# Optimization experiments

Measured on AMD Instinct MI355X. Metric: run time of the kernel, lower is better.

## Reference

```python
import jax, jax.numpy as jnp
import numpy as np

B, NB, T, NC = 32, 55, 512, 8
D, H, E, K, DEPTH, FF = 128, 8, 8, 2, 4, 512  # embed, heads, experts, top_k, depth, ffn hidden=4*D
IN = NB * NC  # 440


def _ln(x, g, b, eps=1e-5):
    m = jnp.mean(x, axis=-1, keepdims=True)
    v = jnp.mean((x - m) ** 2, axis=-1, keepdims=True)
    return (x - m) / jnp.sqrt(v + eps) * g + b


def setup_inputs() -> dict:
    key = jax.random.key(0)
    ks = jax.random.split(key, 16)
    s = 0.02
    return {
        "x": jax.random.normal(ks[0], (B, NB, T, NC), jnp.float32),
        "proj_W": jax.random.normal(ks[1], (IN, D), jnp.float32) * s,
        "proj_b": jnp.zeros((D,), jnp.float32),
        "pos_embed": jax.random.normal(ks[2], (1, T, D), jnp.float32) * s,
        "ln1_g": jnp.ones((DEPTH, D), jnp.float32),
        "ln1_b": jnp.zeros((DEPTH, D), jnp.float32),
        "qkv_W": jax.random.normal(ks[3], (DEPTH, D, 3 * D), jnp.float32) * s,
        "qkv_b": jnp.zeros((DEPTH, 3 * D), jnp.float32),
        "out_W": jax.random.normal(ks[4], (DEPTH, D, D), jnp.float32) * s,
        "out_b": jnp.zeros((DEPTH, D), jnp.float32),
        "ln2_g": jnp.ones((DEPTH, D), jnp.float32),
        "ln2_b": jnp.zeros((DEPTH, D), jnp.float32),
        "gate_W": jax.random.normal(ks[5], (DEPTH, D, E), jnp.float32) * s,
        "w1": jax.random.normal(ks[6], (DEPTH, E, D, FF), jnp.float32) * s,
        "b1": jnp.zeros((DEPTH, E, FF), jnp.float32),
        "w2": jax.random.normal(ks[7], (DEPTH, E, FF, D), jnp.float32) * s,
        "b2": jnp.zeros((DEPTH, E, D), jnp.float32),
        "head_ln_g": jnp.ones((D,), jnp.float32),
        "head_ln_b": jnp.zeros((D,), jnp.float32),
        "head_W": jax.random.normal(ks[8], (D, 2), jnp.float32) * s,
        "head_b": jnp.zeros((2,), jnp.float32),
    }


def reference(x, proj_W, proj_b, pos_embed, ln1_g, ln1_b, qkv_W, qkv_b, out_W,
              out_b, ln2_g, ln2_b, gate_W, w1, b1, w2, b2, head_ln_g,
              head_ln_b, head_W, head_b):
    b, nb, t, nc = x.shape
    h = jnp.transpose(x, (0, 2, 1, 3)).reshape(b, t, nb * nc)  # [b,t,440]
    h = h @ proj_W + proj_b + pos_embed[:, :t, :]
    aux_total = jnp.float32(0.0)
    for i in range(DEPTH):
        # --- pre-LN multi-head self-attention ---
        z = _ln(h, ln1_g[i], ln1_b[i])
        qkv = z @ qkv_W[i] + qkv_b[i]
        q, k, v = jnp.split(qkv, 3, axis=-1)
        dh = D // H
        q = q.reshape(b, t, H, dh)
        k = k.reshape(b, t, H, dh)
        v = v.reshape(b, t, H, dh)
        att = jnp.einsum('bqhd,bkhd->bhqk', q, k) / jnp.sqrt(jnp.float32(dh))
        att = jax.nn.softmax(att, axis=-1)
        o = jnp.einsum('bhqk,bkhd->bqhd', att, v).reshape(b, t, D)
        h = h + o @ out_W[i] + out_b[i]
        # --- pre-LN top-k MoE FFN ---
        z = _ln(h, ln2_g[i], ln2_b[i])
        probs = jax.nn.softmax(z @ gate_W[i], axis=-1)  # [b,t,E]
        topv, topi = jax.lax.top_k(probs, K)
        wts = topv / jnp.sum(topv, axis=-1, keepdims=True)
        combine = jnp.sum(jax.nn.one_hot(topi, E, dtype=probs.dtype) * wts[..., None], axis=-2)  # [b,t,E]
        hid = jax.nn.gelu(jnp.einsum('btd,edf->btef', z, w1[i]) + b1[i])
        yexp = jnp.einsum('btef,efd->bted', hid, w2[i]) + b2[i]
        h = h + jnp.einsum('bte,bted->btd', combine, yexp)
        # Switch-style load-balancing auxiliary loss
        importance = probs.mean(axis=(0, 1))            # mean router prob per expert
        load = (combine > 0).astype(probs.dtype).mean(axis=(0, 1))  # dispatch fraction
        aux_total = aux_total + E * jnp.sum(importance * load)
    pooled = h.mean(axis=1)
    pooled = _ln(pooled, head_ln_g, head_ln_b)
    return pooled @ head_W + head_b, aux_total
```

## Files before the change

kernel.cpp:

```cpp
#include <hip/hip_runtime.h>
#include <hip/hip_bf16.h>
#include <cstdint>
#include <cstddef>

#define BT        16384
#define MAXASSIGN 33792
#define QSCALE    0.36067376022224085f

typedef __attribute__((ext_vector_type(8)))  short short8;
typedef __attribute__((ext_vector_type(4)))  short short4v;
typedef __attribute__((ext_vector_type(4)))  float f32x4;
typedef __attribute__((ext_vector_type(16))) float f32x16;

typedef const uint32_t __attribute__((address_space(1))) gas_u32;
typedef uint32_t __attribute__((address_space(3))) las_u32;

__device__ __forceinline__ void gload16(const void* g, void* l) {
    __builtin_amdgcn_global_load_lds((gas_u32*)g, (las_u32*)l, 16, 0, 0);
}

__device__ __forceinline__ float gelu_f(float x) {
    float u2l = (x + 0.044715f * x * x * x) * 2.3022081927f;
    float e = exp2f(u2l);
    float r = __builtin_amdgcn_rcpf(e + 1.0f);
    return x * e * r;
}

__device__ __forceinline__ unsigned pkbf(float a, float b) {
    __hip_bfloat16 ha = __float2bfloat16(a);
    __hip_bfloat16 hb = __float2bfloat16(b);
    unsigned short ua = *reinterpret_cast<unsigned short*>(&ha);
    unsigned short ub = *reinterpret_cast<unsigned short*>(&hb);
    return (unsigned)ua | ((unsigned)ub << 16);
}

__global__ __launch_bounds__(256) void transpose_kernel(const float* __restrict__ x,
                                                        __hip_bfloat16* __restrict__ xtb) {
    __shared__ unsigned tile[64][228];
    const int b  = blockIdx.x >> 3;
    const int t0 = (blockIdx.x & 7) * 64;
    const int tid = threadIdx.x;
    tile[tid >> 2][220 + (tid & 3)] = 0u;
    const int tt  = tid >> 2;
    const int ncp = tid & 3;
    for (int nb = 0; nb < 55; ++nb) {
        const float2* src = (const float2*)(x + (((size_t)(b * 55 + nb)) * 512 + t0) * 8);
        float2 v = src[tid];
        tile[tt][nb * 4 + ncp] = pkbf(v.x, v.y);
    }
    __syncthreads();
#pragma unroll
    for (int u = 0; u < 14; ++u) {
        int idx = u * 256 + tid;
        int t = idx / 56, c = idx % 56;
        *(uint4*)(xtb + ((size_t)b * 512 + t0 + t) * 448 + c * 8) =
            *(const uint4*)&tile[t][c * 4];
    }
}

__global__ __launch_bounds__(256) void wconvt_kernel(const float* __restrict__ in,
                                                     __hip_bfloat16* __restrict__ out,
                                                     int K, int N) {
    __shared__ float tile[64][65];
    const int kt = K >> 6, nt = N >> 6;
    const int per = kt * nt;
    const int bb  = blockIdx.x / per;
    const int rem = blockIdx.x % per;
    const int k0  = (rem / nt) << 6;
    const int n0  = (rem % nt) << 6;
    const int tid = threadIdx.x;

    const float* src = in + ((size_t)bb * K + k0) * N + n0;
    int tk = tid >> 4;
    int tn = (tid & 15) * 4;
#pragma unroll
    for (int r = 0; r < 4; ++r) {
        float4 v = *(const float4*)(src + (size_t)(tk + r * 16) * N + tn);
        tile[tk + r * 16][tn]     = v.x;
        tile[tk + r * 16][tn + 1] = v.y;
        tile[tk + r * 16][tn + 2] = v.z;
        tile[tk + r * 16][tn + 3] = v.w;
    }
    __syncthreads();
    int on = tid >> 2;
    int ok = (tid & 3) * 16;
    unsigned pk[8];
#pragma unroll
    for (int u = 0; u < 8; ++u)
        pk[u] = pkbf(tile[ok + 2 * u][on], tile[ok + 2 * u + 1][on]);
    uint4* dst = (uint4*)(out + ((size_t)bb * N + n0 + on) * K + k0 + ok);
    dst[0] = (uint4){pk[0], pk[1], pk[2], pk[3]};
    dst[1] = (uint4){pk[4], pk[5], pk[6], pk[7]};
}

__global__ __launch_bounds__(256) void projconv_kernel(const float* __restrict__ in,
                                                       __hip_bfloat16* __restrict__ out) {
    int idx = blockIdx.x * 256 + threadIdx.x;
    int k = idx % 448, n = idx / 448;
    out[idx] = __float2bfloat16(k < 440 ? in[k * 128 + n] : 0.f);
}

template<int MODE, int BM>
__global__ __launch_bounds__(256) void mm_kernel(
    const __hip_bfloat16* __restrict__ A, const __hip_bfloat16* __restrict__ Wt,
    const float* __restrict__ bias, const float* __restrict__ extra,
    void* __restrict__ Cout, int K, int N, int wstride,
    const int* __restrict__ moff, const int* __restrict__ atok,
    const float* __restrict__ awt)
{
    constexpr int FI = BM / 32;
    __shared__ short smem[16384];
    short* As = smem;
    short* Bs = smem + BM * 64;
    const int tid  = threadIdx.x;
    const int row0 = blockIdx.x * BM;
    const int col0 = blockIdx.y * 128;

    const float* bias2 = bias;
    int lim = 0;
    if constexpr (MODE == 3 || MODE == 4) {
        if (row0 >= moff[8]) return;
        int e = 0;
        while (moff[e + 1] <= row0) ++e;
        Wt    += (size_t)e * wstride;
        bias2  = bias + e * N;
        lim    = moff[e] + moff[9 + e];
    }

    const int wave = tid >> 6, lane = tid & 63;
    const int crow = tid >> 3;
    const int cc   = tid & 7;

    int srow[FI];
#pragma unroll
    for (int p = 0; p < FI; ++p) {
        int grow = row0 + p * 32 + crow;
        srow[p] = grow;
        if constexpr (MODE == 3)
            srow[p] = (grow < lim) ? atok[grow] : BT;
    }

    f32x4 acc[FI][4];
#pragma unroll
    for (int i = 0; i < FI; ++i)
#pragma unroll
        for (int j = 0; j < 4; ++j) acc[i][j] = (f32x4){0.f, 0.f, 0.f, 0.f};

    const int wm = (wave >> 1) * (BM / 2), wn = (wave & 1) * 64;
    const int lr = lane & 15, q = lane >> 4;

    for (int k0 = 0; k0 < K; k0 += 64) {
#pragma unroll
        for (int p = 0; p < FI; ++p) {
            int row = p * 32 + crow;
            int sc  = (cc ^ (row & 7)) << 3;
            short* la = &As[(p * 32 + wave * 8) * 64];
            gload16(A + (size_t)srow[p] * K + k0 + sc, la);
        }
#pragma unroll
        for (int p = 0; p < 4; ++p) {
            int row = p * 32 + crow;
            int sc  = (cc ^ (row & 7)) << 3;
            short* lb = &Bs[(p * 32 + wave * 8) * 64];
            gload16(Wt + (size_t)(col0 + row) * K + k0 + sc, lb);
        }
        __syncthreads();
#pragma unroll
        for (int s = 0; s < 2; ++s) {
            short8 af[FI], bf[4];
#pragma unroll
            for (int f = 0; f < FI; ++f) {
                int m = wm + f * 16 + lr;
                af[f] = *(const short8*)&As[(m * 8 + ((s * 4 + q) ^ (m & 7))) * 8];
            }
#pragma unroll
            for (int f = 0; f < 4; ++f) {
                int n = wn + f * 16 + lr;
                bf[f] = *(const short8*)&Bs[(n * 8 + ((s * 4 + q) ^ (n & 7))) * 8];
            }
#pragma unroll
            for (int i = 0; i < FI; ++i)
#pragma unroll
                for (int j = 0; j < 4; ++j)
                    acc[i][j] = __builtin_amdgcn_mfma_f32_16x16x32_bf16(
                        bf[j], af[i], acc[i][j], 0, 0, 0);
        }
        __syncthreads();
    }

    float4 b4[4];
#pragma unroll
    for (int j = 0; j < 4; ++j)
        b4[j] = *(const float4*)&bias2[col0 + wn + j * 16 + q * 4];

    if constexpr (MODE == 3 || MODE == 5) {
        const bool qsc = (MODE == 5) && (col0 == 0);
#pragma unroll
        for (int i = 0; i < FI; ++i) {
            int trow = wm + i * 16 + lr;
#pragma unroll
            for (int j = 0; j < 4; ++j) {
                int cb = wn + j * 16 + q * 4;
                float v0 = acc[i][j][0] + b4[j].x;
                float v1 = acc[i][j][1] + b4[j].y;
                float v2 = acc[i][j][2] + b4[j].z;
                float v3 = acc[i][j][3] + b4[j].w;
                if constexpr (MODE == 3) {
                    v0 = gelu_f(v0); v1 = gelu_f(v1);
                    v2 = gelu_f(v2); v3 = gelu_f(v3);
                }
                if (qsc) { v0 *= QSCALE; v1 *= QSCALE; v2 *= QSCALE; v3 *= QSCALE; }
                uint2 pk = {pkbf(v0, v1), pkbf(v2, v3)};
                int ch = cb >> 3;
                *(uint2*)((char*)smem + trow * 256 + ((ch ^ (trow & 7)) << 4)
                          + ((cb & 7) << 1)) = pk;
            }
        }
        __syncthreads();
        __hip_bfloat16* outb = (__hip_bfloat16*)Cout;
        constexpr int TPR = 256 / BM;
        constexpr int CPT = 16 / TPR;
        int rrow = tid / TPR;
        if constexpr (MODE == 3) {
            size_t rb = (size_t)(row0 + rrow) * N + col0;
#pragma unroll
            for (int u = 0; u < CPT; ++u) {
                int c = (tid % TPR) * CPT + u;
                uint4 d = *(const uint4*)((char*)smem + rrow * 256
                                          + ((c ^ (rrow & 7)) << 4));
                *(uint4*)(outb + rb + c * 8) = d;
            }
        } else {
            size_t pbase = (size_t)(col0 >> 7) * 8 * BT * 16;
#pragma unroll
            for (int u = 0; u < CPT; ++u) {
                int c = (tid % TPR) * CPT + u;
                uint4 d = *(const uint4*)((char*)smem + rrow * 256
                                          + ((c ^ (rrow & 7)) << 4));
                size_t dst = pbase + ((size_t)(c >> 1) * BT + row0 + rrow) * 16
                           + (c & 1) * 8;
                *(uint4*)(outb + dst) = d;
            }
        }
    } else {
        float* outf = (float*)Cout;
        constexpr int HP = BM / 64;
        for (int h = 0; h < HP; ++h) {
            if (HP == 1 || (wm >> 6) == h) {
#pragma unroll
                for (int i = 0; i < FI; ++i) {
                    int trow = (wm & 63) + i * 16 + lr;
#pragma unroll
                    for (int j = 0; j < 4; ++j) {
                        int cb = wn + j * 16 + q * 4;
                        f32x4 v = acc[i][j];
                        v[0] += b4[j].x; v[1] += b4[j].y;
                        v[2] += b4[j].z; v[3] += b4[j].w;
                        int ch = cb >> 2;
                        *(f32x4*)((char*)smem + trow * 512
                                  + ((ch ^ (trow & 7)) << 4)) = v;
                    }
                }
            }
            __syncthreads();
            {
                int rrow = tid >> 2;
                int grow = row0 + h * 64 + rrow;
                float aw = (MODE == 4) ? awt[grow] : 1.f;
                size_t rb = (size_t)grow * N + col0;
#pragma unroll
                for (int u = 0; u < 8; ++u) {
                    int c = (tid & 3) * 8 + u;
                    f32x4 d = *(const f32x4*)((char*)smem + rrow * 512
                                              + ((c ^ (rrow & 7)) << 4));
                    int gcol = col0 + c * 4;
                    if constexpr (MODE == 0) {
                        float4 p = *(const float4*)&extra[(grow & 511) * 128 + gcol];
                        d[0] += p.x; d[1] += p.y; d[2] += p.z; d[3] += p.w;
                    } else if constexpr (MODE == 2) {
                        float4 p = *(const float4*)&extra[rb + c * 4];
                        d[0] += p.x; d[1] += p.y; d[2] += p.z; d[3] += p.w;
                    } else if constexpr (MODE == 4) {
                        d[0] *= aw; d[1] *= aw; d[2] *= aw; d[3] *= aw;
                    }
                    *(f32x4*)&outf[rb + c * 4] = d;
                }
            }
            __syncthreads();
        }
    }
}

__global__ __launch_bounds__(256) void ln_kernel(const float* __restrict__ x,
                                                 const float* __restrict__ g,
                                                 const float* __restrict__ b,
                                                 __hip_bfloat16* __restrict__ zbf) {
    int wave = threadIdx.x >> 6, lane = threadIdx.x & 63;
    size_t row = (size_t)blockIdx.x * 4 + wave;
    const float* xr = x + row * 128;
    float a0 = xr[lane], a1 = xr[lane + 64];
    float s = a0 + a1;
#pragma unroll
    for (int off = 32; off > 0; off >>= 1) s += __shfl_xor(s, off);
    float mean = s * (1.f / 128.f);
    float d0 = a0 - mean, d1 = a1 - mean;
    float v = d0 * d0 + d1 * d1;
#pragma unroll
    for (int off = 32; off > 0; off >>= 1) v += __shfl_xor(v, off);
    float inv = rsqrtf(v * (1.f / 128.f) + 1e-5f);
    zbf[row * 128 + lane]      = __float2bfloat16(d0 * inv * g[lane] + b[lane]);
    zbf[row * 128 + lane + 64] = __float2bfloat16(d1 * inv * g[lane + 64] + b[lane + 64]);
}

__global__ __launch_bounds__(512) void attn_kernel(const __hip_bfloat16* __restrict__ qkv,
                                                   __hip_bfloat16* __restrict__ o) {
    __shared__ short Ks[512 * 24];
    __shared__ short Vt[17 * 520];
    const int b = blockIdx.z, hh = blockIdx.y, half = blockIdx.x;
    const int tid = threadIdx.x;
    const __hip_bfloat16* Qh = qkv + ((size_t)(0 * 8 + hh) * BT + b * 512) * 16;
    const __hip_bfloat16* Kh = qkv + ((size_t)(1 * 8 + hh) * BT + b * 512) * 16;
    const __hip_bfloat16* Vh = qkv + ((size_t)(2 * 8 + hh) * BT + b * 512) * 16;

    {
        int r = tid;
        const uint4* ksrc = (const uint4*)(Kh + (size_t)r * 16);
        uint4 k0 = ksrc[0], k1 = ksrc[1];
        *(uint4*)&Ks[r * 24 + 0] = k0;
        *(uint4*)&Ks[r * 24 + 8] = k1;
        const uint4* vsrc = (const uint4*)(Vh + (size_t)r * 16);
        uint4 v0 = vsrc[0], v1 = vsrc[1];
        unsigned vv[8] = {v0.x, v0.y, v0.z, v0.w, v1.x, v1.y, v1.z, v1.w};
#pragma unroll
        for (int c = 0; c < 8; ++c) {
            Vt[(2 * c)     * 520 + r] = (short)(vv[c] & 0xffff);
            Vt[(2 * c + 1) * 520 + r] = (short)(vv[c] >> 16);
        }
        Vt[16 * 520 + r] = (short)0x3F80;
    }
    __syncthreads();

    const int wave = tid >> 6, lane = tid & 63;
    const int lm = lane & 31, lh = lane >> 5;
    const int qrow0 = half * 256 + wave * 32;

    short8 qf = *(const short8*)(Qh + (size_t)(qrow0 + lm) * 16 + lh * 8);

    f32x16 accO;
#pragma unroll
    for (int r = 0; r < 16; ++r) accO[r] = 0.f;

    for (int kc = 0; kc < 16; ++kc) {
        short8 kf = *(const short8*)&Ks[(kc * 32 + lm) * 24 + lh * 8];
        int vr = (lm < 16) ? lm : 16;
        const short* vb2 = &Vt[vr * 520 + kc * 32];
        short4v va  = *(const short4v*)(vb2 + 4 * lh);
        short4v vbq = *(const short4v*)(vb2 + 8 + 4 * lh);
        short4v vc  = *(const short4v*)(vb2 + 16 + 4 * lh);
        short4v vd  = *(const short4v*)(vb2 + 24 + 4 * lh);
        short8 vf0, vf1;
#pragma unroll
        for (int j = 0; j < 4; ++j) {
            vf0[j] = va[j];  vf0[4 + j] = vbq[j];
            vf1[j] = vc[j];  vf1[4 + j] = vd[j];
        }
        f32x16 st;
#pragma unroll
        for (int r = 0; r < 16; ++r) st[r] = 0.f;
        st = __builtin_amdgcn_mfma_f32_32x32x16_bf16(kf, qf, st, 0, 0, 0);
        short8 pf0, pf1;
#pragma unroll
        for (int r = 0; r < 8; ++r) {
            pf0[r] = (short)(__float_as_uint(exp2f(st[r]))     >> 16);
            pf1[r] = (short)(__float_as_uint(exp2f(st[8 + r])) >> 16);
        }
        accO = __builtin_amdgcn_mfma_f32_32x32x16_bf16(pf0, vf0, accO, 0, 0, 0);
        accO = __builtin_amdgcn_mfma_f32_32x32x16_bf16(pf1, vf1, accO, 0, 0, 0);
    }

#pragma unroll
    for (int r = 0; r < 16; ++r) {
        float val = accO[r];
        float s = __shfl(val, (lane & 32) + 16);
        if (lm < 16) {
            int qr = qrow0 + (r & 3) + 8 * (r >> 2) + 4 * lh;
            o[((size_t)b * 512 + qr) * 128 + hh * 16 + lm] = __float2bfloat16(val / s);
        }
    }
}

__global__ __launch_bounds__(256) void ln2gate_kernel(
    const float* __restrict__ x, const float* __restrict__ g, const float* __restrict__ b,
    const float* __restrict__ gW, __hip_bfloat16* __restrict__ zbf,
    int* __restrict__ topi, float* __restrict__ topw,
    float* __restrict__ impS, int* __restrict__ cntS)
{
    __shared__ float simp[8];
    __shared__ int scnt[8];
    const int tid = threadIdx.x;
    if (tid < 8) { simp[tid] = 0.f; scnt[tid] = 0; }
    __syncthreads();
    const int wave = tid >> 6, lane = tid & 63;
    const size_t row = (size_t)blockIdx.x * 4 + wave;
    const float* xr = x + row * 128;
    float a0 = xr[lane], a1 = xr[lane + 64];
    float s = a0 + a1;
#pragma unroll
    for (int off = 32; off > 0; off >>= 1) s += __shfl_xor(s, off);
    float mean = s * (1.f / 128.f);
    float d0 = a0 - mean, d1 = a1 - mean;
    float v = d0 * d0 + d1 * d1;
#pragma unroll
    for (int off = 32; off > 0; off >>= 1) v += __shfl_xor(v, off);
    float inv = rsqrtf(v * (1.f / 128.f) + 1e-5f);
    float o0 = d0 * inv * g[lane] + b[lane];
    float o1 = d1 * inv * g[lane + 64] + b[lane + 64];
    zbf[row * 128 + lane]      = __float2bfloat16(o0);
    zbf[row * 128 + lane + 64] = __float2bfloat16(o1);
    float4 gA = *(const float4*)&gW[lane * 8];
    float4 gB = *(const float4*)&gW[lane * 8 + 4];
    float4 gC = *(const float4*)&gW[(lane + 64) * 8];
    float4 gD = *(const float4*)&gW[(lane + 64) * 8 + 4];
    float lg[8];
    lg[0] = o0 * gA.x + o1 * gC.x;  lg[1] = o0 * gA.y + o1 * gC.y;
    lg[2] = o0 * gA.z + o1 * gC.z;  lg[3] = o0 * gA.w + o1 * gC.w;
    lg[4] = o0 * gB.x + o1 * gD.x;  lg[5] = o0 * gB.y + o1 * gD.y;
    lg[6] = o0 * gB.z + o1 * gD.z;  lg[7] = o0 * gB.w + o1 * gD.w;
#pragma unroll
    for (int e = 0; e < 8; ++e)
#pragma unroll
        for (int off = 32; off > 0; off >>= 1) lg[e] += __shfl_xor(lg[e], off);
    if (lane == 0) {
        float p[8];
        float mx = lg[0];
#pragma unroll
        for (int k = 1; k < 8; ++k) mx = fmaxf(mx, lg[k]);
        float ssum = 0.f;
#pragma unroll
        for (int k = 0; k < 8; ++k) { p[k] = expf(lg[k] - mx); ssum += p[k]; }
        float pinv = 1.f / ssum;
#pragma unroll
        for (int k = 0; k < 8; ++k) p[k] *= pinv;
        int i0 = 0; float v0 = p[0];
#pragma unroll
        for (int k = 1; k < 8; ++k) if (p[k] > v0) { v0 = p[k]; i0 = k; }
        int i1 = -1; float v1 = -1.f;
#pragma unroll
        for (int k = 0; k < 8; ++k) if (k != i0 && p[k] > v1) { v1 = p[k]; i1 = k; }
        float wsum = v0 + v1;
        topi[row * 2] = i0;  topi[row * 2 + 1] = i1;
        topw[row * 2] = v0 / wsum;  topw[row * 2 + 1] = v1 / wsum;
#pragma unroll
        for (int k = 0; k < 8; ++k) atomicAdd(&simp[k], p[k]);
        atomicAdd(&scnt[i0], 1); atomicAdd(&scnt[i1], 1);
    }
    __syncthreads();
    if (tid < 8) {
        int slot = (blockIdx.x & 63) * 8 + tid;
        atomicAdd(&impS[slot], simp[tid]);
        atomicAdd(&cntS[slot], scnt[tid]);
    }
}

__global__ void offsets_kernel(const int* __restrict__ cntS, const float* __restrict__ impS,
                               int* __restrict__ moff, int* __restrict__ fill,
                               float* __restrict__ aux) {
    __shared__ int   csh[8];
    __shared__ float ish[8];
    const int tid = threadIdx.x;
    const int e = tid & 7, grp = tid >> 3;
    int c = 0; float im = 0.f;
    for (int g = 0; g < 8; ++g) {
        int sl = grp * 8 + g;
        c  += cntS[sl * 8 + e];
        im += impS[sl * 8 + e];
    }
#pragma unroll
    for (int off = 32; off >= 8; off >>= 1) {
        c  += __shfl_down(c, off);
        im += __shfl_down(im, off);
    }
    if (tid < 8) { csh[tid] = c; ish[tid] = im; }
    __syncthreads();
    if (tid == 0) {
        int t = 0; float s = 0.f;
        for (int k = 0; k < 8; ++k) {
            int ck = csh[k];
            moff[k] = t; fill[k] = t;
            moff[9 + k] = ck;
            t += (ck + 127) & ~127;
            s += (ish[k] * (1.f / 16384.f)) * ((float)ck * (1.f / 16384.f));
        }
        moff[8] = t;
        aux[0] += 8.f * s;
    }
}

__global__ __launch_bounds__(256) void scatter_kernel(const int* __restrict__ topi,
                                                      const float* __restrict__ topw,
                                                      int* __restrict__ fill, int* __restrict__ atok,
                                                      float* __restrict__ awt, int* __restrict__ tokpos) {
    __shared__ int lcnt[8];
    __shared__ int lbase[8];
    const int tid = threadIdx.x;
    const int token = blockIdx.x * 256 + tid;
    if (tid < 8) lcnt[tid] = 0;
    __syncthreads();
    const int e0 = topi[token * 2], e1 = topi[token * 2 + 1];
    const float w0 = topw[token * 2], w1 = topw[token * 2 + 1];
    const int l0 = atomicAdd(&lcnt[e0], 1);
    const int l1 = atomicAdd(&lcnt[e1], 1);
    __syncthreads();
    if (tid < 8) lbase[tid] = atomicAdd(&fill[tid], lcnt[tid]);
    __syncthreads();
    const int p0 = lbase[e0] + l0;
    const int p1 = lbase[e1] + l1;
    atok[p0] = token;  awt[p0] = w0;  tokpos[token * 2]     = p0;
    atok[p1] = token;  awt[p1] = w1;  tokpos[token * 2 + 1] = p1;
}

__global__ __launch_bounds__(256) void combine_ln_kernel(
    const float* __restrict__ yw, const int* __restrict__ tokpos,
    float* __restrict__ h, const float* __restrict__ g, const float* __restrict__ b,
    __hip_bfloat16* __restrict__ zbf)
{
    const int tid = threadIdx.x;
    const int wave = tid >> 6, lane = tid & 63;
    const size_t row = (size_t)blockIdx.x * 4 + wave;
    const int p0 = tokpos[row * 2], p1 = tokpos[row * 2 + 1];
    float a0 = h[row * 128 + lane]      + yw[(size_t)p0 * 128 + lane]
             + yw[(size_t)p1 * 128 + lane];
    float a1 = h[row * 128 + lane + 64] + yw[(size_t)p0 * 128 + lane + 64]
             + yw[(size_t)p1 * 128 + lane + 64];
    h[row * 128 + lane]      = a0;
    h[row * 128 + lane + 64] = a1;
    if (zbf) {
        float s = a0 + a1;
#pragma unroll
        for (int off = 32; off > 0; off >>= 1) s += __shfl_xor(s, off);
        float mean = s * (1.f / 128.f);
        float d0 = a0 - mean, d1 = a1 - mean;
        float v = d0 * d0 + d1 * d1;
#pragma unroll
        for (int off = 32; off > 0; off >>= 1) v += __shfl_xor(v, off);
        float inv = rsqrtf(v * (1.f / 128.f) + 1e-5f);
        zbf[row * 128 + lane]      = __float2bfloat16(d0 * inv * g[lane] + b[lane]);
        zbf[row * 128 + lane + 64] = __float2bfloat16(d1 * inv * g[lane + 64] + b[lane + 64]);
    }
}

__global__ __launch_bounds__(1024) void head_kernel(const float* __restrict__ h,
                                                    const float* __restrict__ g,
                                                    const float* __restrict__ bb,
                                                    const float* __restrict__ hW,
                                                    const float* __restrict__ hb,
                                                    const float* __restrict__ aux,
                                                    float* __restrict__ out) {
    __shared__ float part[8][128];
    __shared__ float red[128];
    __shared__ float pl[128];
    int b = blockIdx.x, tid = threadIdx.x;
    int c = tid & 127, w = tid >> 7;
    float s = 0.f;
    for (int t = w; t < 512; t += 8) s += h[((size_t)b * 512 + t) * 128 + c];
    part[w][c] = s;
    __syncthreads();
    float pooled = 0.f;
    if (tid < 128) {
#pragma unroll
        for (int k = 0; k < 8; ++k) pooled += part[k][tid];
        pooled *= (1.f / 512.f);
        red[tid] = pooled;
    }
    __syncthreads();
    for (int st = 64; st > 0; st >>= 1) { if (tid < st) red[tid] += red[tid + st]; __syncthreads(); }
    float mean = red[0] * (1.f / 128.f);
    __syncthreads();
    float d = pooled - mean;
    if (tid < 128) red[tid] = d * d;
    __syncthreads();
    for (int st = 64; st > 0; st >>= 1) { if (tid < st) red[tid] += red[tid + st]; __syncthreads(); }
    float var = red[0] * (1.f / 128.f);
    if (tid < 128) pl[tid] = d / sqrtf(var + 1e-5f) * g[tid] + bb[tid];
    __syncthreads();
    if (tid < 2) {
        float acc = hb[tid];
        for (int k = 0; k < 128; ++k) acc += pl[k] * hW[k * 2 + tid];
        out[b * 2 + tid] = acc;
    }
    if (b == 0 && tid == 0) out[64] = aux[0];
}

extern "C" void kernel_launch(void* const* d_in, const int* in_sizes, int n_in,
                              void* d_out, int out_size, void* d_ws, size_t ws_size,
                              hipStream_t stream) {
    (void)in_sizes; (void)n_in; (void)out_size; (void)ws_size;
    const float* x      = (const float*)d_in[0];
    const float* proj_W = (const float*)d_in[1];
    const float* proj_b = (const float*)d_in[2];
    const float* pos    = (const float*)d_in[3];
    const float* ln1_g  = (const float*)d_in[4];
    const float* ln1_b  = (const float*)d_in[5];
    const float* qkv_W  = (const float*)d_in[6];
    const float* qkv_b  = (const float*)d_in[7];
    const float* out_W  = (const float*)d_in[8];
    const float* out_b  = (const float*)d_in[9];
    const float* ln2_g  = (const float*)d_in[10];
    const float* ln2_b  = (const float*)d_in[11];
    const float* gate_W = (const float*)d_in[12];
    const float* w1     = (const float*)d_in[13];
    const float* b1     = (const float*)d_in[14];
    const float* w2     = (const float*)d_in[15];
    const float* b2     = (const float*)d_in[16];
    const float* hl_g   = (const float*)d_in[17];
    const float* hl_b   = (const float*)d_in[18];
    const float* head_W = (const float*)d_in[19];
    const float* head_b = (const float*)d_in[20];
    float* outp = (float*)d_out;

    float* ws = (float*)d_ws;
    size_t off = 0;
    auto alloc = [&](size_t n) { float* p = ws + off; off += (n + 63) & ~(size_t)63; return p; };
    float* hidbf_f = alloc((size_t)MAXASSIGN * 256);
    float* h       = alloc((size_t)BT * 128);
    float* zbf_f   = alloc((size_t)(BT + 1) * 64);
    float* qkvbf_f = alloc((size_t)BT * 192);
    float* obbf_f  = alloc((size_t)BT * 64);
    float* yw      = alloc((size_t)MAXASSIGN * 128);
    float* projWt_f= alloc(128 * 448 / 2);
    float* qkvWt_f = alloc(4 * 384 * 128 / 2);
    float* outWt_f = alloc(4 * 128 * 128 / 2);
    float* w1t_f   = alloc((size_t)32 * 512 * 128 / 2);
    float* w2t_f   = alloc((size_t)32 * 128 * 512 / 2);
    float* topw    = alloc(32768);
    float* awt     = alloc(MAXASSIGN);
    float* impc    = alloc(4096);
    float* auxp    = alloc(1);
    int* topi      = (int*)alloc(32768);
    int* atok      = (int*)alloc(MAXASSIGN);
    int* tokpos    = (int*)alloc(32768);
    int* moff      = (int*)alloc(32);
    int* fill      = (int*)alloc(8);

    __hip_bfloat16* hidbf  = (__hip_bfloat16*)hidbf_f;
    __hip_bfloat16* xtb    = (__hip_bfloat16*)hidbf_f;
    __hip_bfloat16* zbf    = (__hip_bfloat16*)zbf_f;
    __hip_bfloat16* qkvbf  = (__hip_bfloat16*)qkvbf_f;
    __hip_bfloat16* obbf   = (__hip_bfloat16*)obbf_f;
    __hip_bfloat16* projWt = (__hip_bfloat16*)projWt_f;
    __hip_bfloat16* qkvWt  = (__hip_bfloat16*)qkvWt_f;
    __hip_bfloat16* outWt  = (__hip_bfloat16*)outWt_f;
    __hip_bfloat16* w1t    = (__hip_bfloat16*)w1t_f;
    __hip_bfloat16* w2t    = (__hip_bfloat16*)w2t_f;

    hipMemsetAsync(auxp, 0, 4, stream);
    hipMemsetAsync(impc, 0, 16384, stream);
    hipMemsetAsync((char*)zbf + (size_t)BT * 256, 0, 256, stream);

    transpose_kernel<<<256, 256, 0, stream>>>(x, xtb);
    projconv_kernel<<<224, 256, 0, stream>>>(proj_W, projWt);
    wconvt_kernel<<<48, 256, 0, stream>>>(qkv_W, qkvWt, 128, 384);
    wconvt_kernel<<<16, 256, 0, stream>>>(out_W, outWt, 128, 128);
    wconvt_kernel<<<512, 256, 0, stream>>>(w1, w1t, 128, 512);
    wconvt_kernel<<<512, 256, 0, stream>>>(w2, w2t, 512, 128);

    mm_kernel<0, 64><<<dim3(256, 1), 256, 0, stream>>>(
        xtb, projWt, proj_b, pos, h, 448, 128, 0, nullptr, nullptr, nullptr);
    ln_kernel<<<4096, 256, 0, stream>>>(h, ln1_g, ln1_b, zbf);

    for (int i = 0; i < 4; ++i) {
        float* impS = impc + (size_t)i * 1024;
        int*   cntS = (int*)(impc + (size_t)i * 1024 + 512);
        mm_kernel<5, 64><<<dim3(256, 3), 256, 0, stream>>>(
            zbf, qkvWt + (size_t)i * 384 * 128, qkv_b + i * 384, nullptr, qkvbf,
            128, 384, 0, nullptr, nullptr, nullptr);
        attn_kernel<<<dim3(2, 8, 32), 512, 0, stream>>>(qkvbf, obbf);
        mm_kernel<2, 64><<<dim3(256, 1), 256, 0, stream>>>(
            obbf, outWt + (size_t)i * 128 * 128, out_b + i * 128, h, h,
            128, 128, 0, nullptr, nullptr, nullptr);
        ln2gate_kernel<<<4096, 256, 0, stream>>>(h, ln2_g + i * 128, ln2_b + i * 128,
                                                 gate_W + (size_t)i * 128 * 8, zbf,
                                                 topi, topw, impS, cntS);
        offsets_kernel<<<1, 64, 0, stream>>>(cntS, impS, moff, fill, auxp);
        scatter_kernel<<<64, 256, 0, stream>>>(topi, topw, fill, atok, awt, tokpos);
        mm_kernel<3, 128><<<dim3(264, 4), 256, 0, stream>>>(
            zbf, w1t + (size_t)i * 8 * 512 * 128, b1 + (size_t)i * 8 * 512, nullptr,
            hidbf, 128, 512, 512 * 128, moff, atok, awt);
        mm_kernel<4, 64><<<dim3(528, 1), 256, 0, stream>>>(
            hidbf, w2t + (size_t)i * 8 * 128 * 512, b2 + (size_t)i * 8 * 128, nullptr,
            yw, 512, 128, 128 * 512, moff, atok, awt);
        combine_ln_kernel<<<4096, 256, 0, stream>>>(yw, tokpos, h,
                                                    ln1_g + (i + 1 < 4 ? (i + 1) * 128 : 0),
                                                    ln1_b + (i + 1 < 4 ? (i + 1) * 128 : 0),
                                                    (i < 3) ? zbf : (__hip_bfloat16*)nullptr);
    }
    head_kernel<<<32, 1024, 0, stream>>>(h, hl_g, hl_b, head_W, head_b, auxp, outp);
}
```

Measured before the change: 648.0 us.

## Merge setup kernels and fold offset computation into scatter kernel

Replaces three memsets with a single init kernel, merges the proj-weight conversion into the transpose launch, and merges the four weight transpose launches into one. Each layer's separate offsets kernel is removed. The scatter kernel now derives per-block bases deterministically from per-slot counts, which only works because ln2gate slot indexing was changed to blockIdx>>6 so each slot maps to one scatter block. This cuts launch count and serial tiny kernels, at the cost of every scatter block redundantly reducing the count table.

Result: no change. 639.7 us (-1.3%).

```diff
diff --git a/kernel.cpp b/kernel.cpp
--- a/kernel.cpp
+++ b/kernel.cpp
@@ -34,9 +34,25 @@
     return (unsigned)ua | ((unsigned)ub << 16);
 }
 
+__global__ void init_kernel(float* __restrict__ auxp, float* __restrict__ impc,
+                            unsigned* __restrict__ zrow) {
+    int tid = threadIdx.x;
+    if (tid == 0) auxp[0] = 0.f;
+    for (int u = tid; u < 4096; u += 256) impc[u] = 0.f;
+    if (tid < 64) zrow[tid] = 0u;
+}
+
 __global__ __launch_bounds__(256) void transpose_kernel(const float* __restrict__ x,
-                                                        __hip_bfloat16* __restrict__ xtb) {
+                                                        __hip_bfloat16* __restrict__ xtb,
+                                                        const float* __restrict__ projW,
+                                                        __hip_bfloat16* __restrict__ projWt) {
     __shared__ unsigned tile[64][228];
+    if (blockIdx.x >= 256) {
+        int idx = (blockIdx.x - 256) * 256 + threadIdx.x;
+        int k = idx % 448, n = idx / 448;
+        projWt[idx] = __float2bfloat16(k < 440 ? projW[k * 128 + n] : 0.f);
+        return;
+    }
     const int b  = blockIdx.x >> 3;
     const int t0 = (blockIdx.x & 7) * 64;
     const int tid = threadIdx.x;
@@ -58,14 +74,23 @@
     }
 }
 
-__global__ __launch_bounds__(256) void wconvt_kernel(const float* __restrict__ in,
-                                                     __hip_bfloat16* __restrict__ out,
-                                                     int K, int N) {
+__global__ __launch_bounds__(256) void wconvt4_kernel(
+    const float* __restrict__ qkvW, __hip_bfloat16* __restrict__ qkvWt_,
+    const float* __restrict__ outW, __hip_bfloat16* __restrict__ outWt_,
+    const float* __restrict__ w1i, __hip_bfloat16* __restrict__ w1o,
+    const float* __restrict__ w2i, __hip_bfloat16* __restrict__ w2o)
+{
     __shared__ float tile[64][65];
+    const int bid = blockIdx.x;
+    const float* in; __hip_bfloat16* out; int K, N, blk;
+    if (bid < 48)       { in = qkvW; out = qkvWt_; K = 128; N = 384; blk = bid; }
+    else if (bid < 64)  { in = outW; out = outWt_; K = 128; N = 128; blk = bid - 48; }
+    else if (bid < 576) { in = w1i;  out = w1o;    K = 128; N = 512; blk = bid - 64; }
+    else                { in = w2i;  out = w2o;    K = 512; N = 128; blk = bid - 576; }
     const int kt = K >> 6, nt = N >> 6;
     const int per = kt * nt;
-    const int bb  = blockIdx.x / per;
-    const int rem = blockIdx.x % per;
+    const int bb  = blk / per;
+    const int rem = blk % per;
     const int k0  = (rem / nt) << 6;
     const int n0  = (rem % nt) << 6;
     const int tid = threadIdx.x;
@@ -91,13 +116,6 @@
     uint4* dst = (uint4*)(out + ((size_t)bb * N + n0 + on) * K + k0 + ok);
     dst[0] = (uint4){pk[0], pk[1], pk[2], pk[3]};
     dst[1] = (uint4){pk[4], pk[5], pk[6], pk[7]};
-}
-
-__global__ __launch_bounds__(256) void projconv_kernel(const float* __restrict__ in,
-                                                       __hip_bfloat16* __restrict__ out) {
-    int idx = blockIdx.x * 256 + threadIdx.x;
-    int k = idx % 448, n = idx / 448;
-    out[idx] = __float2bfloat16(k < 440 ? in[k * 128 + n] : 0.f);
 }
 
 template<int MODE, int BM>
@@ -456,63 +474,66 @@
     }
     __syncthreads();
     if (tid < 8) {
-        int slot = (blockIdx.x & 63) * 8 + tid;
+        int slot = (blockIdx.x >> 6) * 8 + tid;
         atomicAdd(&impS[slot], simp[tid]);
         atomicAdd(&cntS[slot], scnt[tid]);
     }
 }
 
-__global__ void offsets_kernel(const int* __restrict__ cntS, const float* __restrict__ impS,
-                               int* __restrict__ moff, int* __restrict__ fill,
-                               float* __restrict__ aux) {
-    __shared__ int   csh[8];
-    __shared__ float ish[8];
+__global__ __launch_bounds__(256) void scatter_kernel(
+    const int* __restrict__ topi, const float* __restrict__ topw,
+    const int* __restrict__ cntS, const float* __restrict__ impS,
+    int* __restrict__ atok, float* __restrict__ awt, int* __restrict__ tokpos,
+    int* __restrict__ moffw, float* __restrict__ aux)
+{
+    __shared__ int lcnt[8];
+    __shared__ int lbase[8];
+    __shared__ int csum[8];
+    __shared__ float isum[8];
     const int tid = threadIdx.x;
-    const int e = tid & 7, grp = tid >> 3;
-    int c = 0; float im = 0.f;
-    for (int g = 0; g < 8; ++g) {
-        int sl = grp * 8 + g;
-        c  += cntS[sl * 8 + e];
-        im += impS[sl * 8 + e];
-    }
-#pragma unroll
-    for (int off = 32; off >= 8; off >>= 1) {
-        c  += __shfl_down(c, off);
-        im += __shfl_down(im, off);
-    }
-    if (tid < 8) { csh[tid] = c; ish[tid] = im; }
-    __syncthreads();
-    if (tid == 0) {
+    const int blk = blockIdx.x;
+    if (tid < 64) {
+        int e = tid & 7, grp = tid >> 3;
+        int ct = 0, cp = 0; float im = 0.f;
+        for (int g = 0; g < 8; ++g) {
+            int sl = grp * 8 + g;
+            int vv = cntS[sl * 8 + e];
+            ct += vv;
+            cp += (sl < blk) ? vv : 0;
+            im += impS[sl * 8 + e];
+        }
+#pragma unroll
+        for (int off = 32; off >= 8; off >>= 1) {
+            ct += __shfl_down(ct, off);
+            cp += __shfl_down(cp, off);
+            im += __shfl_down(im, off);
+        }
+        if (tid < 8) { csum[tid] = ct; isum[tid] = im; lbase[tid] = cp; lcnt[tid] = 0; }
+    }
+    __syncthreads();
+    if (tid < 8) {
+        int t = 0;
+        for (int k = 0; k < tid; ++k) t += (csum[k] + 127) & ~127;
+        lbase[tid] += t;
+    }
+    if (blk == 0 && tid == 64) {
         int t = 0; float s = 0.f;
         for (int k = 0; k < 8; ++k) {
-            int ck = csh[k];
-            moff[k] = t; fill[k] = t;
-            moff[9 + k] = ck;
+            int ck = csum[k];
+            moffw[k] = t;
+            moffw[9 + k] = ck;
             t += (ck + 127) & ~127;
-            s += (ish[k] * (1.f / 16384.f)) * ((float)ck * (1.f / 16384.f));
-        }
-        moff[8] = t;
+            s += (isum[k] * (1.f / 16384.f)) * ((float)ck * (1.f / 16384.f));
+        }
+        moffw[8] = t;
         aux[0] += 8.f * s;
     }
-}
-
-__global__ __launch_bounds__(256) void scatter_kernel(const int* __restrict__ topi,
-                                                      const float* __restrict__ topw,
-                                                      int* __restrict__ fill, int* __restrict__ atok,
-                                                      float* __restrict__ awt, int* __restrict__ tokpos) {
-    __shared__ int lcnt[8];
-    __shared__ int lbase[8];
-    const int tid = threadIdx.x;
-    const int token = blockIdx.x * 256 + tid;
-    if (tid < 8) lcnt[tid] = 0;
-    __syncthreads();
+    __syncthreads();
+    const int token = blk * 256 + tid;
     const int e0 = topi[token * 2], e1 = topi[token * 2 + 1];
     const float w0 = topw[token * 2], w1 = topw[token * 2 + 1];
     const int l0 = atomicAdd(&lcnt[e0], 1);
     const int l1 = atomicAdd(&lcnt[e1], 1);
-    __syncthreads();
-    if (tid < 8) lbase[tid] = atomicAdd(&fill[tid], lcnt[tid]);
-    __syncthreads();
     const int p0 = lbase[e0] + l0;
     const int p1 = lbase[e1] + l1;
     atok[p0] = token;  awt[p0] = w0;  tokpos[token * 2]     = p0;
@@ -640,7 +661,6 @@
     int* atok      = (int*)alloc(MAXASSIGN);
     int* tokpos    = (int*)alloc(32768);
     int* moff      = (int*)alloc(32);
-    int* fill      = (int*)alloc(8);
 
     __hip_bfloat16* hidbf  = (__hip_bfloat16*)hidbf_f;
     __hip_bfloat16* xtb    = (__hip_bfloat16*)hidbf_f;
@@ -653,16 +673,12 @@
     __hip_bfloat16* w1t    = (__hip_bfloat16*)w1t_f;
     __hip_bfloat16* w2t    = (__hip_bfloat16*)w2t_f;
 
-    hipMemsetAsync(auxp, 0, 4, stream);
-    hipMemsetAsync(impc, 0, 16384, stream);
-    hipMemsetAsync((char*)zbf + (size_t)BT * 256, 0, 256, stream);
-
-    transpose_kernel<<<256, 256, 0, stream>>>(x, xtb);
-    projconv_kernel<<<224, 256, 0, stream>>>(proj_W, projWt);
-    wconvt_kernel<<<48, 256, 0, stream>>>(qkv_W, qkvWt, 128, 384);
-    wconvt_kernel<<<16, 256, 0, stream>>>(out_W, outWt, 128, 128);
-    wconvt_kernel<<<512, 256, 0, stream>>>(w1, w1t, 128, 512);
-    wconvt_kernel<<<512, 256, 0, stream>>>(w2, w2t, 512, 128);
+    init_kernel<<<1, 256, 0, stream>>>(auxp, impc,
+                                       (unsigned*)((char*)zbf + (size_t)BT * 256));
+
+    transpose_kernel<<<480, 256, 0, stream>>>(x, xtb, proj_W, projWt);
+    wconvt4_kernel<<<1088, 256, 0, stream>>>(qkv_W, qkvWt, out_W, outWt,
+                                             w1, w1t, w2, w2t);
 
     mm_kernel<0, 64><<<dim3(256, 1), 256, 0, stream>>>(
         xtb, projWt, proj_b, pos, h, 448, 128, 0, nullptr, nullptr, nullptr);
@@ -681,8 +697,8 @@
         ln2gate_kernel<<<4096, 256, 0, stream>>>(h, ln2_g + i * 128, ln2_b + i * 128,
                                                  gate_W + (size_t)i * 128 * 8, zbf,
                                                  topi, topw, impS, cntS);
-        offsets_kernel<<<1, 64, 0, stream>>>(cntS, impS, moff, fill, auxp);
-        scatter_kernel<<<64, 256, 0, stream>>>(topi, topw, fill, atok, awt, tokpos);
+        scatter_kernel<<<64, 256, 0, stream>>>(topi, topw, cntS, impS,
+                                               atok, awt, tokpos, moff, auxp);
         mm_kernel<3, 128><<<dim3(264, 4), 256, 0, stream>>>(
             zbf, w1t + (size_t)i * 8 * 512 * 128, b1 + (size_t)i * 8 * 512, nullptr,
             hidbf, 128, 512, 512 * 128, moff, atok, awt);
```
